# Kernel optimization log

Hardware: AMD Instinct MI355X
Metric: run time of the kernel (lower is better)

## Reference

```python
import jax, jax.numpy as jnp
import numpy as np


def setup_inputs() -> dict:
    key = jax.random.key(0)
    ks = jax.random.split(key, 10)
    B, T = 1024, 8192
    # X features: [time, current I, temperature T, voltage U]
    t = jnp.cumsum(jax.random.uniform(ks[0], (B, T, 1), jnp.float32) + 0.5, axis=1)  # increasing time
    feats = jax.random.normal(ks[1], (B, T, 3), jnp.float32)
    X = jnp.concatenate([t, feats], axis=-1)  # [B, T, 4]
    # SC: [Q (capacity), eta_0, R, SOC_init_base]; keep Q away from 0
    SC = jax.random.uniform(ks[2], (B, 4), jnp.float32, minval=0.5, maxval=1.5)
    std = 0.1
    # SOC_init_net: Linear(4,1) -> Softplus -> Linear(1,1), normal(0,0.1) weights, zero bias
    W1i = jax.random.normal(ks[3], (1, 4), jnp.float32) * std
    b1i = jnp.zeros((1,), jnp.float32)
    W2i = jax.random.normal(ks[4], (1, 1), jnp.float32) * std
    b2i = jnp.zeros((1,), jnp.float32)
    # eta_net: Linear(2,1) -> Softplus -> Linear(1,1)
    W1e = jax.random.normal(ks[5], (1, 2), jnp.float32) * std
    b1e = jnp.zeros((1,), jnp.float32)
    W2e = jax.random.normal(ks[6], (1, 1), jnp.float32) * std
    b2e = jnp.zeros((1,), jnp.float32)
    return {"X": X, "SC": SC, "W1i": W1i, "b1i": b1i, "W2i": W2i, "b2i": b2i,
            "W1e": W1e, "b1e": b1e, "W2e": W2e, "b2e": b2e}


def reference(X, SC, W1i, b1i, W2i, b2i, W1e, b1e, W2e, b2e):
    # X: [B, T, 4] = (t, I, Temp, U); SC: [B, 4] = (Q, eta_0, R, soc_base)
    I = X[..., 1:2]      # [B, T, 1]
    Temp = X[..., 2:3]   # [B, T, 1]
    U = X[..., 3:4]      # [B, T, 1]
    R = SC[..., 2:3]     # [B, 1]
    # SOC_init_net on first-timestep features
    feat0 = jnp.concatenate([I[:, 0, :], Temp[:, 0, :], U[:, 0, :], R], axis=-1)  # [B, 4]
    h0 = jax.nn.softplus(feat0 @ W1i.T + b1i)
    soc_net = h0 @ W2i.T + b2i                     # [B, 1]
    SOC_init = SC[..., 3:4] * (1.0 + soc_net)      # [B, 1]
    # eta_net over all timesteps
    feat = jnp.concatenate([I, Temp], axis=-1)     # [B, T, 2]
    h = jax.nn.softplus(feat @ W1e.T + b1e)
    delta_eta = h @ W2e.T + b2e                    # [B, T, 1]
    # ODE RHS: dSOC/dt = eta_0 * (1 + delta_eta) * I / (3600 * Q)
    Q = SC[..., 0:1][:, None, :]                   # [B, 1, 1]
    eta0 = SC[..., 1:2][:, None, :]                # [B, 1, 1]
    f = eta0 * (1.0 + delta_eta) * I / (3600.0 * Q)  # [B, T, 1]
    # Euler integration: y_{k+1} = y_k + (t_{k+1} - t_k) * f(x_k, y_k); f independent of y -> cumsum
    ts = X[..., 0:1]                               # [B, T, 1]
    dt = ts[:, 1:] - ts[:, :-1]                    # [B, T-1, 1]
    incr = dt * f[:, :-1]                          # [B, T-1, 1]
    zero = jnp.zeros_like(SOC_init)[:, None, :]    # [B, 1, 1]
    SOC = SOC_init[:, None, :] + jnp.concatenate([zero, jnp.cumsum(incr, axis=1)], axis=1)
    return SOC                                     # [B, T, 1]
```

## Files before the change

### kernel.cpp

```cpp
#include <hip/hip_runtime.h>
#include <type_traits>


static __device__ __forceinline__ float bf2f(unsigned int u) {
    union { unsigned int i; float f; } v;
    v.i = u << 16;
    return v.f;
}
static __device__ __forceinline__ unsigned short f2bf(float f) {
    union { unsigned int i; float f; } v;
    v.f = f;
    unsigned int x = v.i;
    return (unsigned short)((x + 0x7fffu + ((x >> 16) & 1u)) >> 16);
}
static __device__ __forceinline__ float sp_fast(float x) {
    return __logf(1.f + __expf(x));
}

struct F4 { float ts, I, Te, U; };
static __device__ __forceinline__ F4 dec(ushort4 x) {
    return {bf2f(x.x), bf2f(x.y), bf2f(x.z), bf2f(x.w)};
}
static __device__ __forceinline__ F4 dec(float4 x) {
    return {x.x, x.y, x.z, x.w};
}

template <bool BF16>
static __device__ __forceinline__ float ld(const void* p, int i) {
    return BF16 ? bf2f(((const unsigned short*)p)[i]) : ((const float*)p)[i];
}

constexpr int BLOCK  = 256;
constexpr int TBLOCK = 512;

__global__ __launch_bounds__(TBLOCK, 8) void socnet_tile(
    const void* __restrict__ Xv, const void* __restrict__ SCv,
    const void* __restrict__ W1iv, const void* __restrict__ b1iv,
    const void* __restrict__ W2iv, const void* __restrict__ b2iv,
    const void* __restrict__ W1ev, const void* __restrict__ b1ev,
    const void* __restrict__ W2ev, const void* __restrict__ b2ev,
    void* __restrict__ outv)
{
    const float* X   = (const float*)Xv;
    const float* SC  = (const float*)SCv;
    const float* W1i = (const float*)W1iv;
    const float* b1i = (const float*)b1iv;
    const float* W2i = (const float*)W2iv;
    const float* b2i = (const float*)b2iv;
    const float* W1e = (const float*)W1ev;
    const float* b1e = (const float*)b1ev;
    const float* W2e = (const float*)W2ev;
    const float* b2e = (const float*)b2ev;

    const int b    = blockIdx.x;
    const int tid  = threadIdx.x;
    const int lane = tid & 63;
    const int wave = tid >> 6;

    const float Q    = SC[b * 4 + 0];
    const float eta0 = SC[b * 4 + 1];
    const float w1e0 = W1e[0];
    const float w1e1 = W1e[1];
    const float vb1e = b1e[0];
    const float coef = eta0 / (3600.f * Q);
    const float c2   = coef * W2e[0];
    const float c1   = coef * (1.f + b2e[0]);

    const float4* Xrow = (const float4*)X + (size_t)b * 8192;
    float4*       orow = (float4*)outv + (size_t)b * 2048;

    __shared__ float s_wt[2][8];
    __shared__ float s_init;

    float carry = 0.f;
    #pragma unroll
    for (int tile = 0; tile < 4; ++tile) {
        const int tbase = tile * 2048;
        const int e0    = tbase + tid * 4;

        const float4 v0 = Xrow[e0 + 0];
        const float4 v1 = Xrow[e0 + 1];
        const float4 v2 = Xrow[e0 + 2];
        const float4 v3 = Xrow[e0 + 3];

        float ts_c, f_c;
        if (tile == 0 && wave == 0) {
            ts_c = v0.x;
            f_c  = 0.f;
        } else {
            const float4 vp = Xrow[tbase + wave * 256 - 1];
            ts_c = vp.x;
            f_c  = fmaf(c2, sp_fast(fmaf(vp.y, w1e0, fmaf(vp.z, w1e1, vb1e))), c1) * vp.y;
        }

        const float f0 = fmaf(c2, sp_fast(fmaf(v0.y, w1e0, fmaf(v0.z, w1e1, vb1e))), c1) * v0.y;
        const float f1 = fmaf(c2, sp_fast(fmaf(v1.y, w1e0, fmaf(v1.z, w1e1, vb1e))), c1) * v1.y;
        const float f2 = fmaf(c2, sp_fast(fmaf(v2.y, w1e0, fmaf(v2.z, w1e1, vb1e))), c1) * v2.y;
        const float f3 = fmaf(c2, sp_fast(fmaf(v3.y, w1e0, fmaf(v3.z, w1e1, vb1e))), c1) * v3.y;

        float pts = __shfl_up(v3.x, 1, 64);
        float pf  = __shfl_up(f3,   1, 64);
        if (lane == 0) { pts = ts_c; pf = f_c; }

        const float g0 = (v0.x - pts) * pf;
        const float g1 = fmaf(v1.x - v0.x, f0, g0);
        const float g2 = fmaf(v2.x - v1.x, f1, g1);
        const float g3 = fmaf(v3.x - v2.x, f2, g2);

        float S = g3;
        #pragma unroll
        for (int d = 1; d < 64; d <<= 1) {
            const float u = __shfl_up(S, d, 64);
            if (lane >= d) S += u;
        }

        if (lane == 63) s_wt[tile & 1][wave] = S;
        if (tile == 0 && tid == 0) {
            const float pre = fmaf(v0.y, W1i[0],
                              fmaf(v0.z, W1i[1],
                              fmaf(v0.w, W1i[2],
                              fmaf(SC[b * 4 + 2], W1i[3], b1i[0]))));
            s_init = SC[b * 4 + 3] *
                     (1.f + fmaf(sp_fast(pre), W2i[0], b2i[0]));
        }
        __syncthreads();

        if (tile == 0) carry = s_init;

        float add = carry + (S - g3);
        #pragma unroll
        for (int w = 0; w < 7; ++w)
            if (w < wave) add += s_wt[tile & 1][w];

        float4 o;
        o.x = g0 + add;
        o.y = g1 + add;
        o.z = g2 + add;
        o.w = g3 + add;
        orow[tile * 512 + tid] = o;

        float wsum = 0.f;
        #pragma unroll
        for (int w = 0; w < 8; ++w)
            wsum += s_wt[tile & 1][w];
        carry += wsum;
    }
}

template <bool BF16>
static __device__ void scan_serial(
    const void* __restrict__ Xv, const void* __restrict__ SCv,
    const void* __restrict__ W1i, const void* __restrict__ b1i,
    const void* __restrict__ W2i, const void* __restrict__ b2i,
    const void* __restrict__ W1e, const void* __restrict__ b1e,
    const void* __restrict__ W2e, const void* __restrict__ b2e,
    void* __restrict__ outv, int T,
    float* s_wts, float* s_wf, float* s_wsum, float* s_carr)
{
    using XVec = typename std::conditional<BF16, ushort4, float4>::type;
    const int b = blockIdx.x, tid = threadIdx.x;
    const int lane = tid & 63, wave = tid >> 6;
    const int ntile = (T + BLOCK - 1) / BLOCK;

    const float Q    = ld<BF16>(SCv, b * 4 + 0);
    const float eta0 = ld<BF16>(SCv, b * 4 + 1);
    const float R    = ld<BF16>(SCv, b * 4 + 2);
    const float S3   = ld<BF16>(SCv, b * 4 + 3);
    const float w1e0 = ld<BF16>(W1e, 0);
    const float w1e1 = ld<BF16>(W1e, 1);
    const float vb1e = ld<BF16>(b1e, 0);
    const float coef = eta0 / (3600.f * Q);
    const float c2   = coef * ld<BF16>(W2e, 0);
    const float c1   = coef * (1.f + ld<BF16>(b2e, 0));

    const XVec* Xrow = (const XVec*)Xv + (size_t)b * T;

    for (int tile = 0; tile < ntile; ++tile) {
        const int t = tile * BLOCK + tid;
        const bool act = t < T;
        F4 v = {0.f, 0.f, 0.f, 0.f};
        if (act) v = dec(Xrow[t]);
        const float f = fmaf(c2, sp_fast(fmaf(v.I, w1e0, fmaf(v.Te, w1e1, vb1e))), c1) * v.I;

        float pts = __shfl_up(v.ts, 1, 64);
        float pf  = __shfl_up(f, 1, 64);

        __syncthreads();
        if (lane == 63) { s_wts[wave] = v.ts; s_wf[wave] = f; }
        if (tile == 0 && tid == 0) {
            const float pre = fmaf(v.I, ld<BF16>(W1i, 0),
                              fmaf(v.Te, ld<BF16>(W1i, 1),
                              fmaf(v.U, ld<BF16>(W1i, 2),
                              fmaf(R, ld<BF16>(W1i, 3), ld<BF16>(b1i, 0)))));
            s_carr[0] = S3 * (1.f + fmaf(sp_fast(pre), ld<BF16>(W2i, 0), ld<BF16>(b2i, 0)));
        }
        __syncthreads();
        if (lane == 0) {
            if (wave == 0) { if (tile > 0) { pts = s_carr[1]; pf = s_carr[2]; } }
            else { pts = s_wts[wave - 1]; pf = s_wf[wave - 1]; }
        }
        float g = (t == 0 || !act) ? 0.f : (v.ts - pts) * pf;
        #pragma unroll
        for (int d = 1; d < 64; d <<= 1) {
            const float u = __shfl_up(g, d, 64);
            if (lane >= d) g += u;
        }
        if (lane == 63) s_wsum[wave] = g;
        __syncthreads();
        float soc = s_carr[0];
        #pragma unroll
        for (int w = 0; w < 3; ++w) if (w < wave) soc += s_wsum[w];
        soc += g;
        if (act) {
            if (BF16) ((unsigned short*)outv)[(size_t)b * T + t] = f2bf(soc);
            else      ((float*)outv)[(size_t)b * T + t] = soc;
        }
        __syncthreads();
        if (tid == BLOCK - 1) { s_carr[0] = soc; s_carr[1] = v.ts; s_carr[2] = f; }
    }
}

__global__ __launch_bounds__(BLOCK) void socnet_serial_k(
    const void* __restrict__ X, const void* __restrict__ SC,
    const void* __restrict__ W1i, const void* __restrict__ b1i,
    const void* __restrict__ W2i, const void* __restrict__ b2i,
    const void* __restrict__ W1e, const void* __restrict__ b1e,
    const void* __restrict__ W2e, const void* __restrict__ b2e,
    void* __restrict__ out, int T)
{
    __shared__ float s_wts[4], s_wf[4], s_wsum[4], s_carr[3];
    const unsigned int* scw = (const unsigned int*)SC;
    const float l0 = bf2f(scw[0] & 0xFFFFu), l1 = bf2f(scw[1] & 0xFFFFu);
    const float l2 = bf2f(scw[2] & 0xFFFFu), l3 = bf2f(scw[3] & 0xFFFFu);
    const bool isbf =
        (l0 >= 0.45f && l0 <= 1.55f) && (l1 >= 0.45f && l1 <= 1.55f) &&
        (l2 >= 0.45f && l2 <= 1.55f) && (l3 >= 0.45f && l3 <= 1.55f);
    if (isbf) scan_serial<true >(X, SC, W1i, b1i, W2i, b2i, W1e, b1e, W2e, b2e,
                                 out, T, s_wts, s_wf, s_wsum, s_carr);
    else      scan_serial<false>(X, SC, W1i, b1i, W2i, b2i, W1e, b1e, W2e, b2e,
                                 out, T, s_wts, s_wf, s_wsum, s_carr);
}

extern "C" void kernel_launch(void* const* d_in, const int* in_sizes, int n_in,
                              void* d_out, int out_size, void* d_ws, size_t ws_size,
                              hipStream_t stream) {
    const int B = in_sizes[1] / 4;
    const int T = in_sizes[0] / (B * 4);

    if (T == 8192) {
        socnet_tile<<<dim3(B), dim3(TBLOCK), 0, stream>>>(
            d_in[0], d_in[1], d_in[2], d_in[3], d_in[4], d_in[5],
            d_in[6], d_in[7], d_in[8], d_in[9], d_out);
    } else {
        socnet_serial_k<<<dim3(B), dim3(BLOCK), 0, stream>>>(
            d_in[0], d_in[1], d_in[2], d_in[3], d_in[4], d_in[5],
            d_in[6], d_in[7], d_in[8], d_in[9], d_out, T);
    }
}
```

Baseline: 218.2 us.

## Give each wave a contiguous row segment and scan it with a single barrier

```diff
diff --git a/kernel.cpp b/kernel.cpp
--- a/kernel.cpp
+++ b/kernel.cpp
@@ -33,7 +33,7 @@
 constexpr int BLOCK  = 256;
 constexpr int TBLOCK = 512;
 
-__global__ __launch_bounds__(TBLOCK, 8) void socnet_tile(
+__global__ __launch_bounds__(TBLOCK, 4) void socnet_full(
     const void* __restrict__ Xv, const void* __restrict__ SCv,
     const void* __restrict__ W1iv, const void* __restrict__ b1iv,
     const void* __restrict__ W2iv, const void* __restrict__ b2iv,
@@ -56,6 +56,7 @@
     const int tid  = threadIdx.x;
     const int lane = tid & 63;
     const int wave = tid >> 6;
+    const int ws   = wave * 1024;
 
     const float Q    = SC[b * 4 + 0];
     const float eta0 = SC[b * 4 + 1];
@@ -67,31 +68,35 @@
     const float c1   = coef * (1.f + b2e[0]);
 
     const float4* Xrow = (const float4*)X + (size_t)b * 8192;
-    float4*       orow = (float4*)outv + (size_t)b * 2048;
-
-    __shared__ float s_wt[2][8];
+
+    float4 ring[16];
+    #pragma unroll
+    for (int c = 0; c < 4; ++c)
+        #pragma unroll
+        for (int j = 0; j < 4; ++j)
+            ring[c * 4 + j] = Xrow[ws + c * 256 + lane * 4 + j];
+
+    float ts_c, f_c;
+    if (wave == 0) {
+        ts_c = ring[0].x;
+        f_c  = 0.f;
+    } else {
+        const float4 vp = Xrow[ws - 1];
+        ts_c = vp.x;
+        f_c  = fmaf(c2, sp_fast(fmaf(vp.y, w1e0, fmaf(vp.z, w1e1, vb1e))), c1) * vp.y;
+    }
+
+    __shared__ float s_wt[8];
     __shared__ float s_init;
 
+    float vals[16];
     float carry = 0.f;
     #pragma unroll
-    for (int tile = 0; tile < 4; ++tile) {
-        const int tbase = tile * 2048;
-        const int e0    = tbase + tid * 4;
-
-        const float4 v0 = Xrow[e0 + 0];
-        const float4 v1 = Xrow[e0 + 1];
-        const float4 v2 = Xrow[e0 + 2];
-        const float4 v3 = Xrow[e0 + 3];
-
-        float ts_c, f_c;
-        if (tile == 0 && wave == 0) {
-            ts_c = v0.x;
-            f_c  = 0.f;
-        } else {
-            const float4 vp = Xrow[tbase + wave * 256 - 1];
-            ts_c = vp.x;
-            f_c  = fmaf(c2, sp_fast(fmaf(vp.y, w1e0, fmaf(vp.z, w1e1, vb1e))), c1) * vp.y;
-        }
+    for (int c = 0; c < 4; ++c) {
+        const float4 v0 = ring[c * 4 + 0];
+        const float4 v1 = ring[c * 4 + 1];
+        const float4 v2 = ring[c * 4 + 2];
+        const float4 v3 = ring[c * 4 + 3];
 
         const float f0 = fmaf(c2, sp_fast(fmaf(v0.y, w1e0, fmaf(v0.z, w1e1, vb1e))), c1) * v0.y;
         const float f1 = fmaf(c2, sp_fast(fmaf(v1.y, w1e0, fmaf(v1.z, w1e1, vb1e))), c1) * v1.y;
@@ -113,37 +118,43 @@
             const float u = __shfl_up(S, d, 64);
             if (lane >= d) S += u;
         }
-
-        if (lane == 63) s_wt[tile & 1][wave] = S;
-        if (tile == 0 && tid == 0) {
-            const float pre = fmaf(v0.y, W1i[0],
-                              fmaf(v0.z, W1i[1],
-                              fmaf(v0.w, W1i[2],
-                              fmaf(SC[b * 4 + 2], W1i[3], b1i[0]))));
-            s_init = SC[b * 4 + 3] *
-                     (1.f + fmaf(sp_fast(pre), W2i[0], b2i[0]));
-        }
-        __syncthreads();
-
-        if (tile == 0) carry = s_init;
-
-        float add = carry + (S - g3);
-        #pragma unroll
-        for (int w = 0; w < 7; ++w)
-            if (w < wave) add += s_wt[tile & 1][w];
-
+        const float tb = carry + (S - g3);
+        vals[c * 4 + 0] = g0 + tb;
+        vals[c * 4 + 1] = g1 + tb;
+        vals[c * 4 + 2] = g2 + tb;
+        vals[c * 4 + 3] = g3 + tb;
+
+        carry += __shfl(S, 63, 64);
+        ts_c   = __shfl(v3.x, 63, 64);
+        f_c    = __shfl(f3, 63, 64);
+    }
+
+    if (lane == 0) s_wt[wave] = carry;
+    if (wave == 0 && lane == 0) {
+        const float4 x0 = ring[0];
+        const float pre = fmaf(x0.y, W1i[0],
+                          fmaf(x0.z, W1i[1],
+                          fmaf(x0.w, W1i[2],
+                          fmaf(SC[b * 4 + 2], W1i[3], b1i[0]))));
+        s_init = SC[b * 4 + 3] *
+                 (1.f + fmaf(sp_fast(pre), W2i[0], b2i[0]));
+    }
+    __syncthreads();
+
+    float base = s_init;
+    #pragma unroll
+    for (int w = 0; w < 7; ++w)
+        if (w < wave) base += s_wt[w];
+
+    float4* orow = (float4*)outv + (size_t)b * 2048 + wave * 256;
+    #pragma unroll
+    for (int c = 0; c < 4; ++c) {
         float4 o;
-        o.x = g0 + add;
-        o.y = g1 + add;
-        o.z = g2 + add;
-        o.w = g3 + add;
-        orow[tile * 512 + tid] = o;
-
-        float wsum = 0.f;
-        #pragma unroll
-        for (int w = 0; w < 8; ++w)
-            wsum += s_wt[tile & 1][w];
-        carry += wsum;
+        o.x = vals[c * 4 + 0] + base;
+        o.y = vals[c * 4 + 1] + base;
+        o.z = vals[c * 4 + 2] + base;
+        o.w = vals[c * 4 + 3] + base;
+        orow[c * 64 + lane] = o;
     }
 }
 
@@ -248,7 +259,7 @@
     const int T = in_sizes[0] / (B * 4);
 
     if (T == 8192) {
-        socnet_tile<<<dim3(B), dim3(TBLOCK), 0, stream>>>(
+        socnet_full<<<dim3(B), dim3(TBLOCK), 0, stream>>>(
             d_in[0], d_in[1], d_in[2], d_in[3], d_in[4], d_in[5],
             d_in[6], d_in[7], d_in[8], d_in[9], d_out);
     } else {
```

Measured after the change: 216.3 us. About the same (-0.9%).
